# Optimization experiments

Measured on AMD Instinct MI355X. Metric: run time of the kernel, lower is better.

The kernel has to match this reference:

```python
import jax, jax.numpy as jnp
import numpy as np
import math

HIDDEN = 128; NHEADS = 4; N_COE = 50; N_SCALES = 4; THRE = 5.0; S = 4096; B = 1


def setup_inputs():
    key = jax.random.key(0)
    ks = jax.random.split(key, 12)
    w = lambda k, shape: jax.random.normal(k, shape, jnp.float32) * 0.05
    return {
        "eigenvalue": jax.random.uniform(ks[0], (B, S), jnp.float32) * 2.0,  # graph Laplacian eigvals in [0,2)
        "length": jnp.full((B,), S, dtype=jnp.int32),
        "sele_num": jnp.full((B,), S, dtype=jnp.int32),
        "eig_w_W": w(ks[1], (HIDDEN + 1, HIDDEN)), "eig_w_b": jnp.zeros((HIDDEN,), jnp.float32),
        "mha_ln_g": jnp.ones((HIDDEN,), jnp.float32), "mha_ln_b": jnp.zeros((HIDDEN,), jnp.float32),
        "in_W": w(ks[2], (HIDDEN, 3 * HIDDEN)), "in_b": jnp.zeros((3 * HIDDEN,), jnp.float32),
        "out_W": w(ks[3], (HIDDEN, HIDDEN)), "out_b": jnp.zeros((HIDDEN,), jnp.float32),
        "ffn_ln_g": jnp.ones((HIDDEN,), jnp.float32), "ffn_ln_b": jnp.zeros((HIDDEN,), jnp.float32),
        "ffn1_W": w(ks[4], (HIDDEN, HIDDEN)), "ffn1_b": jnp.zeros((HIDDEN,), jnp.float32),
        "ffn2_W": w(ks[5], (HIDDEN, HIDDEN)), "ffn2_b": jnp.zeros((HIDDEN,), jnp.float32),
        "dsc_W": w(ks[6], (HIDDEN, N_COE)), "dsc_b": jnp.zeros((N_COE,), jnp.float32),
        "dwv_W": w(ks[7], (HIDDEN, N_COE)), "dwv_b": jnp.zeros((N_COE,), jnp.float32),
        "dss_W": w(ks[8], (HIDDEN, N_SCALES)), "dss_b": jnp.zeros((N_SCALES,), jnp.float32),
    }


def layer_norm(x, g, b, eps=1e-5):
    m = x.mean(-1, keepdims=True)
    v = ((x - m) ** 2).mean(-1, keepdims=True)
    return (x - m) / jnp.sqrt(v + eps) * g + b


def sine_encoding(e, W, b):
    # e: [B, S] -> [B, S, HIDDEN]
    div = jnp.exp(jnp.arange(0, HIDDEN, 2, dtype=e.dtype) * (-math.log(10000.0) / HIDDEN))
    pe = (e * 100.0)[..., None] * div  # [B, S, HIDDEN/2]
    eeig = jnp.concatenate([e[..., None], jnp.sin(pe), jnp.cos(pe)], axis=-1)  # [B, S, HIDDEN+1]
    return eeig @ W + b


def mha(x, pad_mask, in_W, in_b, out_W, out_b):
    # x: [B, S, D]; pad_mask: [B, S] True = masked key
    Bb, Ss, D = x.shape
    hd = D // NHEADS
    qkv = x @ in_W + in_b
    q, k, v = jnp.split(qkv, 3, axis=-1)
    hsplit = lambda t: t.reshape(Bb, Ss, NHEADS, hd).transpose(0, 2, 1, 3)  # [B, H, S, hd]
    q, k, v = hsplit(q), hsplit(k), hsplit(v)
    scores = jnp.einsum('bhqd,bhkd->bhqk', q, k) / math.sqrt(hd)
    scores = jnp.where(pad_mask[:, None, None, :], -jnp.inf, scores)
    attn = jax.nn.softmax(scores, axis=-1)
    o = jnp.einsum('bhqk,bhkd->bhqd', attn, v).transpose(0, 2, 1, 3).reshape(Bb, Ss, D)
    return o @ out_W + out_b


def cheb_base(y, n_coe, flag):
    # Chebyshev recurrence: wavelet = [T_0, T_2, ...], scaling = [T_1, T_3, ...]
    te0 = jnp.ones_like(y)
    to0 = y
    def step(carry, _):
        te, to = carry
        te = 2.0 * y * to - te
        to = 2.0 * y * te - to
        return (te, to), (te, to)
    _, (evens, odds) = jax.lax.scan(step, (te0, to0), None, length=n_coe - 1)
    if flag == 'scaling':
        base = jnp.concatenate([to0[None], odds], axis=0)   # [n_coe, B, S, d]
    else:
        base = jnp.concatenate([te0[None], evens], axis=0)
    return jnp.moveaxis(base, 0, 1)  # [B, n_coe, S, d]


def _forward(eigenvalue, eig_w_W, eig_w_b, mha_ln_g, mha_ln_b, in_W, in_b, out_W, out_b,
             ffn_ln_g, ffn_ln_b, ffn1_W, ffn1_b, ffn2_W, ffn2_b,
             dsc_W, dsc_b, dwv_W, dwv_b, dss_W, dss_b, length, sele_num):
    Bb, Ss = eigenvalue.shape
    eve = eigenvalue
    eig_mask = jnp.arange(Ss)[None, :] >= sele_num[:, None]  # [B, S] True = pad
    # --- EigenEncoding (dropout in eval mode = identity) ---
    eig = sine_encoding(eve, eig_w_W, eig_w_b)
    eig = eig + mha(layer_norm(eig, mha_ln_g, mha_ln_b), eig_mask, in_W, in_b, out_W, out_b)
    f = layer_norm(eig, ffn_ln_g, ffn_ln_b)
    f = jax.nn.gelu(f @ ffn1_W + ffn1_b, approximate=False) @ ffn2_W + ffn2_b
    eig_filter = eig + f  # [B, S, HIDDEN]
    lenf = length.astype(eve.dtype)[:, None]
    def pooled(W, b):
        c = eig_filter @ W + b
        c = jnp.where(eig_mask[..., None], 0.0, c)
        return c.sum(axis=1) / (lenf + 1e-8)
    coe_scaling = jax.nn.sigmoid(pooled(dsc_W, dsc_b))
    coe_scaling = coe_scaling / (coe_scaling.sum(-1, keepdims=True) + 1e-8)  # [B, n_coe]
    coe_wavelet = jax.nn.sigmoid(pooled(dwv_W, dwv_b))
    coe_wavelet = coe_wavelet / (coe_wavelet.sum(-1, keepdims=True) + 1e-8)
    coe_scales = jax.nn.sigmoid(pooled(dss_W, dss_b)) * THRE  # [B, n_scales]
    # --- Chebyshev bases ---
    base_scaling = cheb_base(eve[..., None] - 1.0, N_COE, 'scaling')  # [B, n_coe, S, 1]
    fsw = eve[..., None] * coe_scales[:, None, :]                      # [B, S, n_scales]
    fsw = jnp.where(fsw > 2.0, 0.0, fsw)
    base_wavelet = cheb_base(fsw - 1.0, N_COE, 'wavelet')             # [B, n_coe, S, n_scales]
    base_scaling = 0.5 * (1.0 - base_scaling)
    base_wavelet = 0.5 * (1.0 - base_wavelet)
    curr_scaling = jnp.einsum('bc,bcsd->bsd', coe_scaling, base_scaling)
    curr_wavelet = jnp.einsum('bc,bcsd->bsd', coe_wavelet, base_wavelet)
    out = jnp.concatenate([curr_scaling, curr_wavelet], axis=-1)       # [B, S, 1+n_scales]
    out = out / (jnp.linalg.norm(out, axis=-1, keepdims=True) + 1e-8)  # cfg.lam.tight_use = True
    return out


def reference(eigenvalue, length, sele_num, eig_w_W, eig_w_b, mha_ln_g, mha_ln_b, in_W, in_b,
              out_W, out_b, ffn_ln_g, ffn_ln_b, ffn1_W, ffn1_b, ffn2_W, ffn2_b,
              dsc_W, dsc_b, dwv_W, dwv_b, dss_W, dss_b):
    return _forward(eigenvalue, eig_w_W, eig_w_b, mha_ln_g, mha_ln_b, in_W, in_b, out_W, out_b,
                    ffn_ln_g, ffn_ln_b, ffn1_W, ffn1_b, ffn2_W, ffn2_b,
                    dsc_W, dsc_b, dwv_W, dwv_b, dss_W, dss_b, length, sele_num)
```

## Files before the change

kernel.cpp:

```cpp
#include <hip/hip_runtime.h>
#include <hip/hip_bf16.h>
#include <math.h>


#define KSPLIT 4

typedef __attribute__((ext_vector_type(8))) short short8;
typedef __attribute__((ext_vector_type(4))) float f32x4;

__device__ inline unsigned short f2bf(float x) {
    unsigned u = __float_as_uint(x);
    return (unsigned short)((u + 0x7FFFu + ((u >> 16) & 1u)) >> 16);
}
__device__ inline float bf2f(unsigned short h) { return __uint_as_float(((unsigned)h) << 16); }
__device__ inline unsigned pk_bf16(float lo, float hi) {
    __hip_bfloat162 h = __float22bfloat162_rn(make_float2(lo, hi));
    return *reinterpret_cast<unsigned*>(&h);
}

__global__ __launch_bounds__(512) void k_embed(const float* __restrict__ eve,
    const float* __restrict__ eigW, const float* __restrict__ ebias,
    const float* __restrict__ g, const float* __restrict__ b,
    const float* __restrict__ inW, const float* __restrict__ inb,
    float* __restrict__ eig, float* __restrict__ qkv, unsigned short* __restrict__ Khi_g,
    unsigned short* __restrict__ Klo_g, unsigned short* __restrict__ Vt_g,
    float* __restrict__ xsum)
{
    __shared__ __align__(16) float wsh[2][65 * 128];
    __shared__ __align__(16) float se[16][132];
    __shared__ __align__(16) float xn[16][132];
    __shared__ __align__(16) unsigned short vsh[16][136];
    const int t = threadIdx.x;
    const int r0 = blockIdx.x * 16;
    if (blockIdx.x == 0 && t < 128) xsum[t] = 0.f;

    const float4* __restrict__ eigW4 = (const float4*)eigW;
    const float4* __restrict__ inW4  = (const float4*)inW;
    float4 pf0 = eigW4[t];
    float4 pf1 = eigW4[t + 512];
    float4 pf2 = eigW4[t + 1024];
    float4 pf3 = eigW4[t + 1536];
    float4 pf4;
    if (t < 32) pf4 = eigW4[t + 2048];

    {
        const int rr = t >> 5, l5 = t & 31;
        const float e = eve[r0 + rr];
        if (l5 == 0) se[rr][128] = e;
        #pragma unroll
        for (int jj = 0; jj < 2; ++jj) {
            const int j = l5 * 2 + jj;
            const float div = __expf(-0.07195578415606394f * (float)(2 * j));
            const float pe = e * 100.0f * div;
            se[rr][j]      = __sinf(pe);
            se[rr][64 + j] = __cosf(pe);
        }
    }
    {
        float4* dst = (float4*)wsh[0];
        dst[t] = pf0; dst[t + 512] = pf1; dst[t + 1024] = pf2; dst[t + 1536] = pf3;
        if (t < 32) dst[t + 2048] = pf4;
    }
    const int r  = t >> 5;
    const int c0 = (t & 31) * 4;
    const int kb = t >> 5, c4 = t & 31;
    float a0, a1, a2, a3;
    float xa[4];

    __syncthreads();
    pf0 = eigW4[2080 + t];        pf1 = eigW4[2080 + t + 512];
    pf2 = eigW4[2080 + t + 1024]; pf3 = eigW4[2080 + t + 1536];
    {
        const float* __restrict__ W = wsh[0];
        const float4 w0 = *(const float4*)&W[c0];
        const float ea = se[r][128];
        a0 = ea * w0.x; a1 = ea * w0.y; a2 = ea * w0.z; a3 = ea * w0.w;
        #pragma unroll 8
        for (int k = 0; k < 64; ++k) {
            const float xv = se[r][k];
            const float4 wk = *(const float4*)&W[(k + 1) * 128 + c0];
            a0 = fmaf(xv, wk.x, a0); a1 = fmaf(xv, wk.y, a1);
            a2 = fmaf(xv, wk.z, a2); a3 = fmaf(xv, wk.w, a3);
        }
    }
    {   float4* dst = (float4*)wsh[1];
        dst[t] = pf0; dst[t + 512] = pf1; dst[t + 1024] = pf2; dst[t + 1536] = pf3;
    }
    __syncthreads();
    pf0 = inW4[(size_t)(kb +  0) * 96 + c4];
    pf1 = inW4[(size_t)(kb + 16) * 96 + c4];
    pf2 = inW4[(size_t)(kb + 32) * 96 + c4];
    pf3 = inW4[(size_t)(kb + 48) * 96 + c4];
    {
        const float* __restrict__ W = wsh[1];
        #pragma unroll 8
        for (int k = 64; k < 128; ++k) {
            const float xv = se[r][k];
            const float4 wk = *(const float4*)&W[(k - 64) * 128 + c0];
            a0 = fmaf(xv, wk.x, a0); a1 = fmaf(xv, wk.y, a1);
            a2 = fmaf(xv, wk.z, a2); a3 = fmaf(xv, wk.w, a3);
        }
        const float4 bb = *(const float4*)&ebias[c0];
        xa[0] = a0 + bb.x; xa[1] = a1 + bb.y; xa[2] = a2 + bb.z; xa[3] = a3 + bb.w;
        *(float4*)&eig[(size_t)(r0 + r) * 128 + c0] = make_float4(xa[0], xa[1], xa[2], xa[3]);
        float sa = (xa[0] + xa[1]) + (xa[2] + xa[3]);
        float qa = (xa[0] * xa[0] + xa[1] * xa[1]) + (xa[2] * xa[2] + xa[3] * xa[3]);
        #pragma unroll
        for (int m = 1; m < 32; m <<= 1) {
            sa += __shfl_xor(sa, m, 32); qa += __shfl_xor(qa, m, 32);
        }
        const float ma = sa * (1.f / 128.f);
        const float ia = 1.f / sqrtf(qa * (1.f / 128.f) - ma * ma + 1e-5f);
        const float4 gg = *(const float4*)&g[c0];
        const float4 lb = *(const float4*)&b[c0];
        *(float4*)&xn[r][c0] = make_float4((xa[0] - ma) * ia * gg.x + lb.x,
                                           (xa[1] - ma) * ia * gg.y + lb.y,
                                           (xa[2] - ma) * ia * gg.z + lb.z,
                                           (xa[3] - ma) * ia * gg.w + lb.w);
    }
    {   float4* dst = (float4*)wsh[0];
        dst[t] = pf0; dst[t + 512] = pf1; dst[t + 1024] = pf2; dst[t + 1536] = pf3;
    }
    const int row = r0 + r;
    float A0, A1, A2, A3;
    #pragma unroll
    for (int p = 0; p < 3; ++p) {
        #pragma unroll
        for (int hh = 0; hh < 2; ++hh) {
            __syncthreads();
            const bool last = (p == 2 && hh == 1);
            if (!last) {
                const int np = p + hh, nh = hh ^ 1;
                pf0 = inW4[(size_t)(kb +  0 + nh * 64) * 96 + np * 32 + c4];
                pf1 = inW4[(size_t)(kb + 16 + nh * 64) * 96 + np * 32 + c4];
                pf2 = inW4[(size_t)(kb + 32 + nh * 64) * 96 + np * 32 + c4];
                pf3 = inW4[(size_t)(kb + 48 + nh * 64) * 96 + np * 32 + c4];
            }
            if (hh == 0) {
                const float4 bb = *(const float4*)&inb[p * 128 + c0];
                A0 = bb.x; A1 = bb.y; A2 = bb.z; A3 = bb.w;
            }
            const float* __restrict__ W = wsh[hh];
            #pragma unroll 8
            for (int k2 = 0; k2 < 64; ++k2) {
                const float xv = xn[r][hh * 64 + k2];
                const float4 wk = *(const float4*)&W[k2 * 128 + c0];
                A0 = fmaf(xv, wk.x, A0); A1 = fmaf(xv, wk.y, A1);
                A2 = fmaf(xv, wk.z, A2); A3 = fmaf(xv, wk.w, A3);
            }
            if (!last) {
                float4* dst = (float4*)wsh[hh ^ 1];
                dst[t] = pf0; dst[t + 512] = pf1; dst[t + 1024] = pf2; dst[t + 1536] = pf3;
            }
            if (hh == 1) {
                if (p == 0) {
                    *(float4*)&qkv[(size_t)row * 384 + c0] = make_float4(A0, A1, A2, A3);
                } else if (p == 1) {
                    const int h = c0 >> 5, d = c0 & 31;
                    float A[4] = {A0, A1, A2, A3};
                    unsigned short h4[4], l4v[4];
                    #pragma unroll
                    for (int i = 0; i < 4; ++i) { h4[i] = f2bf(A[i]); l4v[i] = f2bf(A[i] - bf2f(h4[i])); }
                    *(uint2*)&Khi_g[((size_t)h * 4096 + row) * 32 + d] = *(uint2*)h4;
                    *(uint2*)&Klo_g[((size_t)h * 4096 + row) * 32 + d] = *(uint2*)l4v;
                } else {
                    unsigned short v4[4];
                    float A[4] = {A0, A1, A2, A3};
                    #pragma unroll
                    for (int i = 0; i < 4; ++i) v4[i] = f2bf(A[i]);
                    *(uint2*)&vsh[r][c0] = *(uint2*)v4;
                }
            }
        }
    }
    __syncthreads();
    if (t < 128) {
        __align__(16) unsigned short tmp[16];
        #pragma unroll
        for (int k2 = 0; k2 < 16; ++k2) tmp[k2] = vsh[k2][t];
        *(uint4*)&Vt_g[(size_t)t * 4096 + r0]     = *(uint4*)&tmp[0];
        *(uint4*)&Vt_g[(size_t)t * 4096 + r0 + 8] = *(uint4*)&tmp[8];
    }
}

#define KSTR 40
#define VSTR 72
#define PSTR 72

__global__ __launch_bounds__(256) void k_attn(const float* __restrict__ qkv,
    const unsigned short* __restrict__ Khi_g, const unsigned short* __restrict__ Klo_g,
    const unsigned short* __restrict__ Vt_g,
    const int* __restrict__ sele, float* __restrict__ Oe, float* __restrict__ E)
{
    __shared__ __align__(16) unsigned short Khi[2][64 * KSTR];
    __shared__ __align__(16) unsigned short Klo[2][64 * KSTR];
    __shared__ __align__(16) unsigned short Vt[2][32 * VSTR];
    __shared__ __align__(16) unsigned short Pb[4][16 * PSTR];

    const int t = threadIdx.x;
    const int lane = t & 63;
    const int l = lane & 15;
    const int quad = lane >> 4;
    const int wv = __builtin_amdgcn_readfirstlane(t >> 6);
    const int qb = blockIdx.x;
    const int h  = blockIdx.y;
    const int ks = blockIdx.z;
    const int nk = sele[0];

    short8 qhi, qlo;
    {
        const float* __restrict__ qr = qkv + (size_t)(qb * 64 + wv * 16 + l) * 384 + h * 32 + quad * 8;
        const float4 a = *(const float4*)qr;
        const float4 b = *(const float4*)(qr + 4);
        const float sc = 0.17677669529663687f;
        float v[8] = {a.x * sc, a.y * sc, a.z * sc, a.w * sc, b.x * sc, b.y * sc, b.z * sc, b.w * sc};
        #pragma unroll
        for (int j = 0; j < 8; ++j) {
            const unsigned short hb = f2bf(v[j]);
            qhi[j] = (short)hb;
            qlo[j] = (short)f2bf(v[j] - bf2f(hb));
        }
    }
    f32x4 accO0 = {0.f, 0.f, 0.f, 0.f};
    f32x4 accO1 = {0.f, 0.f, 0.f, 0.f};
    float elane = 0.f;

    const int kk = t >> 2;
    const int d0 = (t & 3) * 8;
    const int vd = t >> 3;
    const int ko = (t & 7) * 8;

    const unsigned short* __restrict__ pKhi = Khi_g + ((size_t)h * 4096 + ks * 1024 + kk) * 32 + d0;
    const unsigned short* __restrict__ pKlo = Klo_g + ((size_t)h * 4096 + ks * 1024 + kk) * 32 + d0;
    const unsigned short* __restrict__ pVt  = Vt_g  + ((size_t)h * 32 + vd) * 4096 + ks * 1024 + ko;

    uint4 kh_n = *(const uint4*)pKhi;
    uint4 kl_n = *(const uint4*)pKlo;
    uint4 vv_n = *(const uint4*)pVt;
    *(uint4*)&Khi[0][kk * KSTR + d0] = kh_n;
    *(uint4*)&Klo[0][kk * KSTR + d0] = kl_n;
    *(uint4*)&Vt[0][vd * VSTR + ko]  = vv_n;

    for (int ch = 0; ch < 16; ++ch) {
        __syncthreads();
        const int cur = ch & 1;
        if (ch < 15) {
            kh_n = *(const uint4*)(pKhi + (size_t)(ch + 1) * 2048);
            kl_n = *(const uint4*)(pKlo + (size_t)(ch + 1) * 2048);
            vv_n = *(const uint4*)(pVt  + (ch + 1) * 64);
        }
        const int keybase = ks * 1024 + ch * 64;
        const unsigned short* __restrict__ KhiC = Khi[cur];
        const unsigned short* __restrict__ KloC = Klo[cur];
        const unsigned short* __restrict__ VtC  = Vt[cur];
        unsigned short* __restrict__ Pw = Pb[wv];
        #pragma unroll
        for (int tile = 0; tile < 4; ++tile) {
            const int kl = tile * 16 + l;
            const short8 kh = *(const short8*)&KhiC[kl * KSTR + quad * 8];
            const short8 kw = *(const short8*)&KloC[kl * KSTR + quad * 8];
            f32x4 S = {0.f, 0.f, 0.f, 0.f};
            __builtin_amdgcn_s_setprio(1);
            S = __builtin_amdgcn_mfma_f32_16x16x32_bf16(kh, qhi, S, 0, 0, 0);
            S = __builtin_amdgcn_mfma_f32_16x16x32_bf16(kw, qhi, S, 0, 0, 0);
            S = __builtin_amdgcn_mfma_f32_16x16x32_bf16(kh, qlo, S, 0, 0, 0);
            __builtin_amdgcn_s_setprio(0);
            const int kg0 = keybase + tile * 16 + quad * 4;
            const float p0 = (kg0 + 0 < nk) ? __expf(S[0]) : 0.f;
            const float p1 = (kg0 + 1 < nk) ? __expf(S[1]) : 0.f;
            const float p2 = (kg0 + 2 < nk) ? __expf(S[2]) : 0.f;
            const float p3 = (kg0 + 3 < nk) ? __expf(S[3]) : 0.f;
            elane += (p0 + p1) + (p2 + p3);
            *(uint2*)&Pw[l * PSTR + tile * 16 + quad * 4] =
                make_uint2(pk_bf16(p0, p1), pk_bf16(p2, p3));
        }
        #pragma unroll
        for (int step = 0; step < 2; ++step) {
            const short8 pa  = *(const short8*)&Pw[l * PSTR + step * 32 + quad * 8];
            const short8 vb0 = *(const short8*)&VtC[l * VSTR + step * 32 + quad * 8];
            const short8 vb1 = *(const short8*)&VtC[(16 + l) * VSTR + step * 32 + quad * 8];
            __builtin_amdgcn_s_setprio(1);
            accO0 = __builtin_amdgcn_mfma_f32_16x16x32_bf16(pa, vb0, accO0, 0, 0, 0);
            accO1 = __builtin_amdgcn_mfma_f32_16x16x32_bf16(pa, vb1, accO1, 0, 0, 0);
            __builtin_amdgcn_s_setprio(0);
        }
        if (ch < 15) {
            *(uint4*)&Khi[cur ^ 1][kk * KSTR + d0] = kh_n;
            *(uint4*)&Klo[cur ^ 1][kk * KSTR + d0] = kl_n;
            *(uint4*)&Vt[cur ^ 1][vd * VSTR + ko]  = vv_n;
        }
    }
    elane += __shfl_xor(elane, 16, 64);
    elane += __shfl_xor(elane, 32, 64);
    const int qrow0 = qb * 64 + wv * 16;
    if (lane < 16)
        E[((size_t)ks * 4 + h) * 4096 + qrow0 + l] = elane;
    #pragma unroll
    for (int r = 0; r < 4; ++r) {
        const size_t row = qrow0 + quad * 4 + r;
        Oe[((size_t)ks * 4096 + row) * 128 + h * 32 + l]      = accO0[r];
        Oe[((size_t)ks * 4096 + row) * 128 + h * 32 + 16 + l] = accO1[r];
    }
}

__global__ __launch_bounds__(512) void k_ffn(const float* __restrict__ eig,
    const float* __restrict__ Oe, const float* __restrict__ E,
    const float* __restrict__ outW, const float* __restrict__ outb,
    const float* __restrict__ lg, const float* __restrict__ lb,
    const float* __restrict__ W1, const float* __restrict__ b1,
    const float* __restrict__ W2, const float* __restrict__ b2,
    const int* __restrict__ sele, float* __restrict__ xsum)
{
    __shared__ __align__(16) float wsh[2][64 * 128];
    __shared__ __align__(16) float sA[16][132];
    __shared__ __align__(16) float xn[16][132];
    __shared__ __align__(16) float cs[16][132];
    const int t = threadIdx.x;
    const int r0 = blockIdx.x * 16;
    const int r  = t >> 5;
    const int c0 = (t & 31) * 4;

    const float4* __restrict__ Wp0 = (const float4*)outW;
    const float4* __restrict__ Wp1 = (const float4*)W1;
    const float4* __restrict__ Wp2 = (const float4*)W2;

    float4 pf0 = Wp0[t], pf1 = Wp0[t + 512], pf2 = Wp0[t + 1024], pf3 = Wp0[t + 1536];

    {
        const int h = c0 >> 5;
        float es = 0.f;
        float v[4] = {0.f, 0.f, 0.f, 0.f};
        #pragma unroll
        for (int ks = 0; ks < KSPLIT; ++ks) {
            es += E[((size_t)ks * 4 + h) * 4096 + r0 + r];
            const float4 o1 = *(const float4*)&Oe[((size_t)ks * 4096 + r0 + r) * 128 + c0];
            v[0] += o1.x; v[1] += o1.y; v[2] += o1.z; v[3] += o1.w;
        }
        const float rcp = 1.f / es;
        *(float4*)&sA[r][c0] = make_float4(v[0] * rcp, v[1] * rcp, v[2] * rcp, v[3] * rcp);
    }
    {   float4* dst = (float4*)wsh[0];
        dst[t] = pf0; dst[t + 512] = pf1; dst[t + 1024] = pf2; dst[t + 1536] = pf3;
    }

    float x2[4];
    float A0, A1, A2, A3;
    #pragma unroll
    for (int gphase = 0; gphase < 6; ++gphase) {
        const int gg = gphase >> 1, hh = gphase & 1;
        __syncthreads();
        if (gphase < 5) {
            const int nid = gphase + 1;
            const int ng = nid >> 1, nh = nid & 1;
            const float4* __restrict__ src = (ng == 0) ? Wp0 : (ng == 1 ? Wp1 : Wp2);
            pf0 = src[nh * 2048 + t];        pf1 = src[nh * 2048 + t + 512];
            pf2 = src[nh * 2048 + t + 1024]; pf3 = src[nh * 2048 + t + 1536];
        }
        if (hh == 0) {
            const float* bias = (gg == 0) ? outb : (gg == 1 ? b1 : b2);
            const float4 bb = *(const float4*)&bias[c0];
            A0 = bb.x; A1 = bb.y; A2 = bb.z; A3 = bb.w;
        }
        const float* __restrict__ W = wsh[hh];
        const float* __restrict__ act = (gg == 1) ? &xn[r][0] : &sA[r][0];
        #pragma unroll 8
        for (int k2 = 0; k2 < 64; ++k2) {
            const float xv = act[hh * 64 + k2];
            const float4 wk = *(const float4*)&W[k2 * 128 + c0];
            A0 = fmaf(xv, wk.x, A0); A1 = fmaf(xv, wk.y, A1);
            A2 = fmaf(xv, wk.z, A2); A3 = fmaf(xv, wk.w, A3);
        }
        if (gphase < 5) {
            float4* dst = (float4*)wsh[hh ^ 1];
            dst[t] = pf0; dst[t + 512] = pf1; dst[t + 1024] = pf2; dst[t + 1536] = pf3;
        }
        if (hh == 1) {
            if (gg == 0) {
                const float4 ea = *(const float4*)&eig[(size_t)(r0 + r) * 128 + c0];
                x2[0] = ea.x + A0; x2[1] = ea.y + A1; x2[2] = ea.z + A2; x2[3] = ea.w + A3;
                float sa = (x2[0] + x2[1]) + (x2[2] + x2[3]);
                float qa = (x2[0] * x2[0] + x2[1] * x2[1]) + (x2[2] * x2[2] + x2[3] * x2[3]);
                #pragma unroll
                for (int m = 1; m < 32; m <<= 1) {
                    sa += __shfl_xor(sa, m, 32); qa += __shfl_xor(qa, m, 32);
                }
                const float ma = sa * (1.f / 128.f);
                const float ia = 1.f / sqrtf(qa * (1.f / 128.f) - ma * ma + 1e-5f);
                const float4 gg4 = *(const float4*)&lg[c0];
                const float4 bb4 = *(const float4*)&lb[c0];
                *(float4*)&xn[r][c0] = make_float4((x2[0] - ma) * ia * gg4.x + bb4.x,
                                                   (x2[1] - ma) * ia * gg4.y + bb4.y,
                                                   (x2[2] - ma) * ia * gg4.z + bb4.z,
                                                   (x2[3] - ma) * ia * gg4.w + bb4.w);
            } else if (gg == 1) {
                *(float4*)&sA[r][c0] = make_float4(
                    0.5f * A0 * (1.f + erff(A0 * 0.70710678118654752f)),
                    0.5f * A1 * (1.f + erff(A1 * 0.70710678118654752f)),
                    0.5f * A2 * (1.f + erff(A2 * 0.70710678118654752f)),
                    0.5f * A3 * (1.f + erff(A3 * 0.70710678118654752f)));
            } else {
                const int nsel = sele[0];
                const bool ina = (r0 + r) < nsel;
                *(float4*)&cs[r][c0] = ina ? make_float4(x2[0] + A0, x2[1] + A1, x2[2] + A2, x2[3] + A3)
                                           : make_float4(0.f, 0.f, 0.f, 0.f);
            }
        }
    }
    __syncthreads();
    if (t < 128) {
        float s = 0.f;
        #pragma unroll
        for (int rr = 0; rr < 16; ++rr) s += cs[rr][t];
        atomicAdd(&xsum[t], s);
    }
}

__global__ __launch_bounds__(128) void k_tail(const float* __restrict__ eve,
    const float* __restrict__ xsum,
    const float* __restrict__ dscW, const float* __restrict__ dscb,
    const float* __restrict__ dwvW, const float* __restrict__ dwvb,
    const float* __restrict__ dssW, const float* __restrict__ dssb,
    const int* __restrict__ len, const int* __restrict__ sele,
    float* __restrict__ out)
{
    __shared__ float xs[128];
    __shared__ float val[104];
    __shared__ float s2[2];
    __shared__ float csc[50], cwv[50], cssh[4];
    const int t = threadIdx.x;
    xs[t] = xsum[t];
    __syncthreads();
    if (t < 104) {
        const float invl = 1.f / ((float)len[0] + 1e-8f);
        const float ns = (float)sele[0];
        const float* Wp; int stride, col; float bias;
        if (t < 50)       { Wp = dscW; stride = 50; col = t;       bias = dscb[t]; }
        else if (t < 100) { Wp = dwvW; stride = 50; col = t - 50;  bias = dwvb[t - 50]; }
        else              { Wp = dssW; stride = 4;  col = t - 100; bias = dssb[t - 100]; }
        float a = 0.f;
        #pragma unroll 4
        for (int k = 0; k < 128; ++k) a = fmaf(xs[k], Wp[k * stride + col], a);
        a = (a + ns * bias) * invl;
        val[t] = 1.f / (1.f + __expf(-a));
    }
    __syncthreads();
    if (t == 0) { float s = 0.f; for (int i = 0; i < 50; ++i) s += val[i]; s2[0] = s; }
    if (t == 1) { float s = 0.f; for (int i = 0; i < 50; ++i) s += val[50 + i]; s2[1] = s; }
    __syncthreads();
    if (t < 50) {
        csc[t] = val[t] / (s2[0] + 1e-8f);
        cwv[t] = val[50 + t] / (s2[1] + 1e-8f);
    } else if (t >= 100 && t < 104) {
        cssh[t - 100] = val[t] * 5.0f;
    }
    __syncthreads();
    const int s = blockIdx.x * 128 + t;
    const float e = eve[s];
    float vals[5];
    {
        const float y = e - 1.f;
        float te = 1.f, to = y;
        float a = csc[0] * (0.5f * (1.f - to));
        const float y2 = 2.f * y;
        for (int i = 1; i < 50; ++i) {
            te = fmaf(y2, to, -te);
            to = fmaf(y2, te, -to);
            a = fmaf(csc[i], 0.5f * (1.f - to), a);
        }
        vals[0] = a;
    }
    #pragma unroll
    for (int j = 0; j < 4; ++j) {
        float f = e * cssh[j];
        if (f > 2.f) f = 0.f;
        const float y = f - 1.f;
        float te = 1.f, to = y;
        float a = cwv[0] * (0.5f * (1.f - te));
        const float y2 = 2.f * y;
        for (int i = 1; i < 50; ++i) {
            te = fmaf(y2, to, -te);
            to = fmaf(y2, te, -to);
            a = fmaf(cwv[i], 0.5f * (1.f - te), a);
        }
        vals[1 + j] = a;
    }
    float n2 = 0.f;
    #pragma unroll
    for (int k = 0; k < 5; ++k) n2 += vals[k] * vals[k];
    const float invn = 1.f / (sqrtf(n2) + 1e-8f);
    #pragma unroll
    for (int k = 0; k < 5; ++k) out[s * 5 + k] = vals[k] * invn;
}

extern "C" void kernel_launch(void* const* d_in, const int* in_sizes, int n_in,
                              void* d_out, int out_size, void* d_ws, size_t ws_size,
                              hipStream_t stream) {
    const float* eve  = (const float*)d_in[0];
    const int*   len  = (const int*)d_in[1];
    const int*   sele = (const int*)d_in[2];
    const float* eigW = (const float*)d_in[3];
    const float* eigB = (const float*)d_in[4];
    const float* mlg  = (const float*)d_in[5];
    const float* mlb  = (const float*)d_in[6];
    const float* inW  = (const float*)d_in[7];
    const float* inb  = (const float*)d_in[8];
    const float* outW = (const float*)d_in[9];
    const float* outb = (const float*)d_in[10];
    const float* flg  = (const float*)d_in[11];
    const float* flb  = (const float*)d_in[12];
    const float* W1   = (const float*)d_in[13];
    const float* b1   = (const float*)d_in[14];
    const float* W2   = (const float*)d_in[15];
    const float* b2   = (const float*)d_in[16];
    const float* dscW = (const float*)d_in[17];
    const float* dscb = (const float*)d_in[18];
    const float* dwvW = (const float*)d_in[19];
    const float* dwvb = (const float*)d_in[20];
    const float* dssW = (const float*)d_in[21];
    const float* dssb = (const float*)d_in[22];

    float* ws   = (float*)d_ws;
    float* eig  = ws;
    float* qkv  = ws + 524288;
    float* Oe   = ws + 2097152;
    float* E    = ws + 4194304;
    float* xsum = ws + 4259840;
    unsigned short* Khi_g = (unsigned short*)(ws + 4260352);
    unsigned short* Klo_g = (unsigned short*)(ws + 4522496);
    unsigned short* Vt_g  = (unsigned short*)(ws + 4784640);
    float* out  = (float*)d_out;

    k_embed<<<256, 512, 0, stream>>>(eve, eigW, eigB, mlg, mlb, inW, inb,
                                     eig, qkv, Khi_g, Klo_g, Vt_g, xsum);
    k_attn <<<dim3(64, 4, KSPLIT), 256, 0, stream>>>(qkv, Khi_g, Klo_g, Vt_g, sele, Oe, E);
    k_ffn  <<<256, 512, 0, stream>>>(eig, Oe, E, outW, outb, flg, flb, W1, b1, W2, b2, sele, xsum);
    k_tail <<<32, 128, 0, stream>>>(eve, xsum, dscW, dscb, dwvW, dwvb, dssW, dssb, len, sele, out);
}
```

Baseline: 180.6 us.

## Compute two rows per thread in embed/FFN GEMVs and spread tail over more blocks

k_embed and k_ffn drop from 512 to 256 threads per block, and each thread now accumulates two rows. Every shared-memory weight float4 load is reused for two rows, which halves LDS weight traffic per FMA, at the cost of more registers and fewer waves. k_tail goes from 32 to 256 blocks, and each thread now computes one of the five Chebyshev series for one eigenvalue instead of all five. This spreads the serial 50-step recurrences across many more threads, but every block repeats the small coefficient MLP prologue.

```diff
diff --git a/kernel.cpp b/kernel.cpp
--- a/kernel.cpp
+++ b/kernel.cpp
@@ -18,7 +18,7 @@
     return *reinterpret_cast<unsigned*>(&h);
 }
 
-__global__ __launch_bounds__(512) void k_embed(const float* __restrict__ eve,
+__global__ __launch_bounds__(256) void k_embed(const float* __restrict__ eve,
     const float* __restrict__ eigW, const float* __restrict__ ebias,
     const float* __restrict__ g, const float* __restrict__ b,
     const float* __restrict__ inW, const float* __restrict__ inb,
@@ -36,20 +36,18 @@
 
     const float4* __restrict__ eigW4 = (const float4*)eigW;
     const float4* __restrict__ inW4  = (const float4*)inW;
-    float4 pf0 = eigW4[t];
-    float4 pf1 = eigW4[t + 512];
-    float4 pf2 = eigW4[t + 1024];
-    float4 pf3 = eigW4[t + 1536];
-    float4 pf4;
-    if (t < 32) pf4 = eigW4[t + 2048];
+    float4 pf[8]; float4 pfx;
+    #pragma unroll
+    for (int i = 0; i < 8; ++i) pf[i] = eigW4[t + i * 256];
+    if (t < 32) pfx = eigW4[t + 2048];
 
     {
-        const int rr = t >> 5, l5 = t & 31;
+        const int rr = t >> 4, l4 = t & 15;
         const float e = eve[r0 + rr];
-        if (l5 == 0) se[rr][128] = e;
-        #pragma unroll
-        for (int jj = 0; jj < 2; ++jj) {
-            const int j = l5 * 2 + jj;
+        if (l4 == 0) se[rr][128] = e;
+        #pragma unroll
+        for (int jj = 0; jj < 4; ++jj) {
+            const int j = l4 * 4 + jj;
             const float div = __expf(-0.07195578415606394f * (float)(2 * j));
             const float pe = e * 100.0f * div;
             se[rr][j]      = __sinf(pe);
@@ -58,71 +56,92 @@
     }
     {
         float4* dst = (float4*)wsh[0];
-        dst[t] = pf0; dst[t + 512] = pf1; dst[t + 1024] = pf2; dst[t + 1536] = pf3;
-        if (t < 32) dst[t + 2048] = pf4;
-    }
-    const int r  = t >> 5;
-    const int c0 = (t & 31) * 4;
+        #pragma unroll
+        for (int i = 0; i < 8; ++i) dst[t + i * 256] = pf[i];
+        if (t < 32) dst[t + 2048] = pfx;
+    }
+    const int lane = t & 63;
+    const int w = t >> 6;
+    const int rp = w * 2 + (lane >> 5);
+    const int c0 = (lane & 31) * 4;
+    const int ra = rp * 2, rb = ra + 1;
     const int kb = t >> 5, c4 = t & 31;
-    float a0, a1, a2, a3;
-    float xa[4];
-
-    __syncthreads();
-    pf0 = eigW4[2080 + t];        pf1 = eigW4[2080 + t + 512];
-    pf2 = eigW4[2080 + t + 1024]; pf3 = eigW4[2080 + t + 1536];
+    float a0, a1, a2, a3, b0, b1, b2, b3;
+    float xa[4], xb[4];
+
+    __syncthreads();
+    #pragma unroll
+    for (int i = 0; i < 8; ++i) pf[i] = eigW4[2080 + t + i * 256];
     {
         const float* __restrict__ W = wsh[0];
         const float4 w0 = *(const float4*)&W[c0];
-        const float ea = se[r][128];
+        const float ea = se[ra][128], eb = se[rb][128];
         a0 = ea * w0.x; a1 = ea * w0.y; a2 = ea * w0.z; a3 = ea * w0.w;
+        b0 = eb * w0.x; b1 = eb * w0.y; b2 = eb * w0.z; b3 = eb * w0.w;
         #pragma unroll 8
         for (int k = 0; k < 64; ++k) {
-            const float xv = se[r][k];
+            const float xva = se[ra][k];
+            const float xvb = se[rb][k];
             const float4 wk = *(const float4*)&W[(k + 1) * 128 + c0];
-            a0 = fmaf(xv, wk.x, a0); a1 = fmaf(xv, wk.y, a1);
-            a2 = fmaf(xv, wk.z, a2); a3 = fmaf(xv, wk.w, a3);
+            a0 = fmaf(xva, wk.x, a0); a1 = fmaf(xva, wk.y, a1);
+            a2 = fmaf(xva, wk.z, a2); a3 = fmaf(xva, wk.w, a3);
+            b0 = fmaf(xvb, wk.x, b0); b1 = fmaf(xvb, wk.y, b1);
+            b2 = fmaf(xvb, wk.z, b2); b3 = fmaf(xvb, wk.w, b3);
         }
     }
     {   float4* dst = (float4*)wsh[1];
-        dst[t] = pf0; dst[t + 512] = pf1; dst[t + 1024] = pf2; dst[t + 1536] = pf3;
-    }
-    __syncthreads();
-    pf0 = inW4[(size_t)(kb +  0) * 96 + c4];
-    pf1 = inW4[(size_t)(kb + 16) * 96 + c4];
-    pf2 = inW4[(size_t)(kb + 32) * 96 + c4];
-    pf3 = inW4[(size_t)(kb + 48) * 96 + c4];
+        #pragma unroll
+        for (int i = 0; i < 8; ++i) dst[t + i * 256] = pf[i];
+    }
+    __syncthreads();
+    #pragma unroll
+    for (int i = 0; i < 8; ++i) pf[i] = inW4[(size_t)(kb + 8 * i) * 96 + c4];
     {
         const float* __restrict__ W = wsh[1];
         #pragma unroll 8
-        for (int k = 64; k < 128; ++k) {
-            const float xv = se[r][k];
-            const float4 wk = *(const float4*)&W[(k - 64) * 128 + c0];
-            a0 = fmaf(xv, wk.x, a0); a1 = fmaf(xv, wk.y, a1);
-            a2 = fmaf(xv, wk.z, a2); a3 = fmaf(xv, wk.w, a3);
+        for (int k2 = 0; k2 < 64; ++k2) {
+            const float xva = se[ra][64 + k2];
+            const float xvb = se[rb][64 + k2];
+            const float4 wk = *(const float4*)&W[k2 * 128 + c0];
+            a0 = fmaf(xva, wk.x, a0); a1 = fmaf(xva, wk.y, a1);
+            a2 = fmaf(xva, wk.z, a2); a3 = fmaf(xva, wk.w, a3);
+            b0 = fmaf(xvb, wk.x, b0); b1 = fmaf(xvb, wk.y, b1);
+            b2 = fmaf(xvb, wk.z, b2); b3 = fmaf(xvb, wk.w, b3);
         }
         const float4 bb = *(const float4*)&ebias[c0];
         xa[0] = a0 + bb.x; xa[1] = a1 + bb.y; xa[2] = a2 + bb.z; xa[3] = a3 + bb.w;
-        *(float4*)&eig[(size_t)(r0 + r) * 128 + c0] = make_float4(xa[0], xa[1], xa[2], xa[3]);
+        xb[0] = b0 + bb.x; xb[1] = b1 + bb.y; xb[2] = b2 + bb.z; xb[3] = b3 + bb.w;
+        *(float4*)&eig[(size_t)(r0 + ra) * 128 + c0] = make_float4(xa[0], xa[1], xa[2], xa[3]);
+        *(float4*)&eig[(size_t)(r0 + rb) * 128 + c0] = make_float4(xb[0], xb[1], xb[2], xb[3]);
         float sa = (xa[0] + xa[1]) + (xa[2] + xa[3]);
         float qa = (xa[0] * xa[0] + xa[1] * xa[1]) + (xa[2] * xa[2] + xa[3] * xa[3]);
+        float sb = (xb[0] + xb[1]) + (xb[2] + xb[3]);
+        float qb = (xb[0] * xb[0] + xb[1] * xb[1]) + (xb[2] * xb[2] + xb[3] * xb[3]);
         #pragma unroll
         for (int m = 1; m < 32; m <<= 1) {
             sa += __shfl_xor(sa, m, 32); qa += __shfl_xor(qa, m, 32);
-        }
-        const float ma = sa * (1.f / 128.f);
+            sb += __shfl_xor(sb, m, 32); qb += __shfl_xor(qb, m, 32);
+        }
+        const float ma = sa * (1.f / 128.f), mb = sb * (1.f / 128.f);
         const float ia = 1.f / sqrtf(qa * (1.f / 128.f) - ma * ma + 1e-5f);
+        const float ib = 1.f / sqrtf(qb * (1.f / 128.f) - mb * mb + 1e-5f);
         const float4 gg = *(const float4*)&g[c0];
         const float4 lb = *(const float4*)&b[c0];
-        *(float4*)&xn[r][c0] = make_float4((xa[0] - ma) * ia * gg.x + lb.x,
-                                           (xa[1] - ma) * ia * gg.y + lb.y,
-                                           (xa[2] - ma) * ia * gg.z + lb.z,
-                                           (xa[3] - ma) * ia * gg.w + lb.w);
+        *(float4*)&xn[ra][c0] = make_float4((xa[0] - ma) * ia * gg.x + lb.x,
+                                            (xa[1] - ma) * ia * gg.y + lb.y,
+                                            (xa[2] - ma) * ia * gg.z + lb.z,
+                                            (xa[3] - ma) * ia * gg.w + lb.w);
+        *(float4*)&xn[rb][c0] = make_float4((xb[0] - mb) * ib * gg.x + lb.x,
+                                            (xb[1] - mb) * ib * gg.y + lb.y,
+                                            (xb[2] - mb) * ib * gg.z + lb.z,
+                                            (xb[3] - mb) * ib * gg.w + lb.w);
     }
     {   float4* dst = (float4*)wsh[0];
-        dst[t] = pf0; dst[t + 512] = pf1; dst[t + 1024] = pf2; dst[t + 1536] = pf3;
-    }
-    const int row = r0 + r;
-    float A0, A1, A2, A3;
+        #pragma unroll
+        for (int i = 0; i < 8; ++i) dst[t + i * 256] = pf[i];
+    }
+    const int rowa = r0 + ra, rowb = r0 + rb;
+    float A[4], Bv[4];
     #pragma unroll
     for (int p = 0; p < 3; ++p) {
         #pragma unroll
@@ -131,44 +150,54 @@
             const bool last = (p == 2 && hh == 1);
             if (!last) {
                 const int np = p + hh, nh = hh ^ 1;
-                pf0 = inW4[(size_t)(kb +  0 + nh * 64) * 96 + np * 32 + c4];
-                pf1 = inW4[(size_t)(kb + 16 + nh * 64) * 96 + np * 32 + c4];
-                pf2 = inW4[(size_t)(kb + 32 + nh * 64) * 96 + np * 32 + c4];
-                pf3 = inW4[(size_t)(kb + 48 + nh * 64) * 96 + np * 32 + c4];
+                #pragma unroll
+                for (int i = 0; i < 8; ++i)
+                    pf[i] = inW4[(size_t)(kb + 8 * i + nh * 64) * 96 + np * 32 + c4];
             }
             if (hh == 0) {
                 const float4 bb = *(const float4*)&inb[p * 128 + c0];
-                A0 = bb.x; A1 = bb.y; A2 = bb.z; A3 = bb.w;
+                A[0] = bb.x; A[1] = bb.y; A[2] = bb.z; A[3] = bb.w;
+                Bv[0] = bb.x; Bv[1] = bb.y; Bv[2] = bb.z; Bv[3] = bb.w;
             }
             const float* __restrict__ W = wsh[hh];
             #pragma unroll 8
             for (int k2 = 0; k2 < 64; ++k2) {
-                const float xv = xn[r][hh * 64 + k2];
+                const float xva = xn[ra][hh * 64 + k2];
+                const float xvb = xn[rb][hh * 64 + k2];
                 const float4 wk = *(const float4*)&W[k2 * 128 + c0];
-                A0 = fmaf(xv, wk.x, A0); A1 = fmaf(xv, wk.y, A1);
-                A2 = fmaf(xv, wk.z, A2); A3 = fmaf(xv, wk.w, A3);
+                A[0] = fmaf(xva, wk.x, A[0]); A[1] = fmaf(xva, wk.y, A[1]);
+                A[2] = fmaf(xva, wk.z, A[2]); A[3] = fmaf(xva, wk.w, A[3]);
+                Bv[0] = fmaf(xvb, wk.x, Bv[0]); Bv[1] = fmaf(xvb, wk.y, Bv[1]);
+                Bv[2] = fmaf(xvb, wk.z, Bv[2]); Bv[3] = fmaf(xvb, wk.w, Bv[3]);
             }
             if (!last) {
                 float4* dst = (float4*)wsh[hh ^ 1];
-                dst[t] = pf0; dst[t + 512] = pf1; dst[t + 1024] = pf2; dst[t + 1536] = pf3;
+                #pragma unroll
+                for (int i = 0; i < 8; ++i) dst[t + i * 256] = pf[i];
             }
             if (hh == 1) {
                 if (p == 0) {
-                    *(float4*)&qkv[(size_t)row * 384 + c0] = make_float4(A0, A1, A2, A3);
+                    *(float4*)&qkv[(size_t)rowa * 384 + c0] = make_float4(A[0], A[1], A[2], A[3]);
+                    *(float4*)&qkv[(size_t)rowb * 384 + c0] = make_float4(Bv[0], Bv[1], Bv[2], Bv[3]);
                 } else if (p == 1) {
                     const int h = c0 >> 5, d = c0 & 31;
-                    float A[4] = {A0, A1, A2, A3};
                     unsigned short h4[4], l4v[4];
                     #pragma unroll
                     for (int i = 0; i < 4; ++i) { h4[i] = f2bf(A[i]); l4v[i] = f2bf(A[i] - bf2f(h4[i])); }
-                    *(uint2*)&Khi_g[((size_t)h * 4096 + row) * 32 + d] = *(uint2*)h4;
-                    *(uint2*)&Klo_g[((size_t)h * 4096 + row) * 32 + d] = *(uint2*)l4v;
+                    *(uint2*)&Khi_g[((size_t)h * 4096 + rowa) * 32 + d] = *(uint2*)h4;
+                    *(uint2*)&Klo_g[((size_t)h * 4096 + rowa) * 32 + d] = *(uint2*)l4v;
+                    #pragma unroll
+                    for (int i = 0; i < 4; ++i) { h4[i] = f2bf(Bv[i]); l4v[i] = f2bf(Bv[i] - bf2f(h4[i])); }
+                    *(uint2*)&Khi_g[((size_t)h * 4096 + rowb) * 32 + d] = *(uint2*)h4;
+                    *(uint2*)&Klo_g[((size_t)h * 4096 + rowb) * 32 + d] = *(uint2*)l4v;
                 } else {
                     unsigned short v4[4];
-                    float A[4] = {A0, A1, A2, A3};
                     #pragma unroll
                     for (int i = 0; i < 4; ++i) v4[i] = f2bf(A[i]);
-                    *(uint2*)&vsh[r][c0] = *(uint2*)v4;
+                    *(uint2*)&vsh[ra][c0] = *(uint2*)v4;
+                    #pragma unroll
+                    for (int i = 0; i < 4; ++i) v4[i] = f2bf(Bv[i]);
+                    *(uint2*)&vsh[rb][c0] = *(uint2*)v4;
                 }
             }
         }
@@ -303,7 +332,7 @@
     }
 }
 
-__global__ __launch_bounds__(512) void k_ffn(const float* __restrict__ eig,
+__global__ __launch_bounds__(256) void k_ffn(const float* __restrict__ eig,
     const float* __restrict__ Oe, const float* __restrict__ E,
     const float* __restrict__ outW, const float* __restrict__ outb,
     const float* __restrict__ lg, const float* __restrict__ lb,
@@ -317,34 +346,44 @@
     __shared__ __align__(16) float cs[16][132];
     const int t = threadIdx.x;
     const int r0 = blockIdx.x * 16;
-    const int r  = t >> 5;
-    const int c0 = (t & 31) * 4;
+    const int lane = t & 63;
+    const int w = t >> 6;
+    const int rp = w * 2 + (lane >> 5);
+    const int c0 = (lane & 31) * 4;
+    const int ra = rp * 2, rb = ra + 1;
 
     const float4* __restrict__ Wp0 = (const float4*)outW;
     const float4* __restrict__ Wp1 = (const float4*)W1;
     const float4* __restrict__ Wp2 = (const float4*)W2;
 
-    float4 pf0 = Wp0[t], pf1 = Wp0[t + 512], pf2 = Wp0[t + 1024], pf3 = Wp0[t + 1536];
+    float4 pf[8];
+    #pragma unroll
+    for (int i = 0; i < 8; ++i) pf[i] = Wp0[t + i * 256];
 
     {
-        const int h = c0 >> 5;
+        const int r = t >> 4, c8 = (t & 15) * 8;
+        const int h = c8 >> 5;
         float es = 0.f;
-        float v[4] = {0.f, 0.f, 0.f, 0.f};
+        float v[8] = {0.f, 0.f, 0.f, 0.f, 0.f, 0.f, 0.f, 0.f};
         #pragma unroll
         for (int ks = 0; ks < KSPLIT; ++ks) {
             es += E[((size_t)ks * 4 + h) * 4096 + r0 + r];
-            const float4 o1 = *(const float4*)&Oe[((size_t)ks * 4096 + r0 + r) * 128 + c0];
+            const float4 o1 = *(const float4*)&Oe[((size_t)ks * 4096 + r0 + r) * 128 + c8];
+            const float4 o2 = *(const float4*)&Oe[((size_t)ks * 4096 + r0 + r) * 128 + c8 + 4];
             v[0] += o1.x; v[1] += o1.y; v[2] += o1.z; v[3] += o1.w;
+            v[4] += o2.x; v[5] += o2.y; v[6] += o2.z; v[7] += o2.w;
         }
         const float rcp = 1.f / es;
-        *(float4*)&sA[r][c0] = make_float4(v[0] * rcp, v[1] * rcp, v[2] * rcp, v[3] * rcp);
+        *(float4*)&sA[r][c8]     = make_float4(v[0] * rcp, v[1] * rcp, v[2] * rcp, v[3] * rcp);
+        *(float4*)&sA[r][c8 + 4] = make_float4(v[4] * rcp, v[5] * rcp, v[6] * rcp, v[7] * rcp);
     }
     {   float4* dst = (float4*)wsh[0];
-        dst[t] = pf0; dst[t + 512] = pf1; dst[t + 1024] = pf2; dst[t + 1536] = pf3;
-    }
-
-    float x2[4];
-    float A0, A1, A2, A3;
+        #pragma unroll
+        for (int i = 0; i < 8; ++i) dst[t + i * 256] = pf[i];
+    }
+
+    float x2a[4], x2b[4];
+    float A[4], Bv[4];
     #pragma unroll
     for (int gphase = 0; gphase < 6; ++gphase) {
         const int gg = gphase >> 1, hh = gphase & 1;
@@ -353,56 +392,81 @@
             const int nid = gphase + 1;
             const int ng = nid >> 1, nh = nid & 1;
             const float4* __restrict__ src = (ng == 0) ? Wp0 : (ng == 1 ? Wp1 : Wp2);
-            pf0 = src[nh * 2048 + t];        pf1 = src[nh * 2048 + t + 512];
-            pf2 = src[nh * 2048 + t + 1024]; pf3 = src[nh * 2048 + t + 1536];
+            #pragma unroll
+            for (int i = 0; i < 8; ++i) pf[i] = src[nh * 2048 + t + i * 256];
         }
         if (hh == 0) {
             const float* bias = (gg == 0) ? outb : (gg == 1 ? b1 : b2);
             const float4 bb = *(const float4*)&bias[c0];
-            A0 = bb.x; A1 = bb.y; A2 = bb.z; A3 = bb.w;
+            A[0] = bb.x; A[1] = bb.y; A[2] = bb.z; A[3] = bb.w;
+            Bv[0] = bb.x; Bv[1] = bb.y; Bv[2] = bb.z; Bv[3] = bb.w;
         }
         const float* __restrict__ W = wsh[hh];
-        const float* __restrict__ act = (gg == 1) ? &xn[r][0] : &sA[r][0];
+        const float* __restrict__ actA = (gg == 1) ? &xn[ra][0] : &sA[ra][0];
+        const float* __restrict__ actB = (gg == 1) ? &xn[rb][0] : &sA[rb][0];
         #pragma unroll 8
         for (int k2 = 0; k2 < 64; ++k2) {
-            const float xv = act[hh * 64 + k2];
+            const float xva = actA[hh * 64 + k2];
+            const float xvb = actB[hh * 64 + k2];
             const float4 wk = *(const float4*)&W[k2 * 128 + c0];
-            A0 = fmaf(xv, wk.x, A0); A1 = fmaf(xv, wk.y, A1);
-            A2 = fmaf(xv, wk.z, A2); A3 = fmaf(xv, wk.w, A3);
+            A[0] = fmaf(xva, wk.x, A[0]); A[1] = fmaf(xva, wk.y, A[1]);
+            A[2] = fmaf(xva, wk.z, A[2]); A[3] = fmaf(xva, wk.w, A[3]);
+            Bv[0] = fmaf(xvb, wk.x, Bv[0]); Bv[1] = fmaf(xvb, wk.y, Bv[1]);
+            Bv[2] = fmaf(xvb, wk.z, Bv[2]); Bv[3] = fmaf(xvb, wk.w, Bv[3]);
         }
         if (gphase < 5) {
             float4* dst = (float4*)wsh[hh ^ 1];
-            dst[t] = pf0; dst[t + 512] = pf1; dst[t + 1024] = pf2; dst[t + 1536] = pf3;
+            #pragma unroll
+            for (int i = 0; i < 8; ++i) dst[t + i * 256] = pf[i];
         }
         if (hh == 1) {
             if (gg == 0) {
-                const float4 ea = *(const float4*)&eig[(size_t)(r0 + r) * 128 + c0];
-                x2[0] = ea.x + A0; x2[1] = ea.y + A1; x2[2] = ea.z + A2; x2[3] = ea.w + A3;
-                float sa = (x2[0] + x2[1]) + (x2[2] + x2[3]);
-                float qa = (x2[0] * x2[0] + x2[1] * x2[1]) + (x2[2] * x2[2] + x2[3] * x2[3]);
+                const float4 ea = *(const float4*)&eig[(size_t)(r0 + ra) * 128 + c0];
+                const float4 eb = *(const float4*)&eig[(size_t)(r0 + rb) * 128 + c0];
+                x2a[0] = ea.x + A[0]; x2a[1] = ea.y + A[1]; x2a[2] = ea.z + A[2]; x2a[3] = ea.w + A[3];
+                x2b[0] = eb.x + Bv[0]; x2b[1] = eb.y + Bv[1]; x2b[2] = eb.z + Bv[2]; x2b[3] = eb.w + Bv[3];
+                float sa = (x2a[0] + x2a[1]) + (x2a[2] + x2a[3]);
+                float qa = (x2a[0] * x2a[0] + x2a[1] * x2a[1]) + (x2a[2] * x2a[2] + x2a[3] * x2a[3]);
+                float sb = (x2b[0] + x2b[1]) + (x2b[2] + x2b[3]);
+                float qb = (x2b[0] * x2b[0] + x2b[1] * x2b[1]) + (x2b[2] * x2b[2] + x2b[3] * x2b[3]);
                 #pragma unroll
                 for (int m = 1; m < 32; m <<= 1) {
                     sa += __shfl_xor(sa, m, 32); qa += __shfl_xor(qa, m, 32);
+                    sb += __shfl_xor(sb, m, 32); qb += __shfl_xor(qb, m, 32);
                 }
-                const float ma = sa * (1.f / 128.f);
+                const float ma = sa * (1.f / 128.f), mb = sb * (1.f / 128.f);
                 const float ia = 1.f / sqrtf(qa * (1.f / 128.f) - ma * ma + 1e-5f);
+                const float ib = 1.f / sqrtf(qb * (1.f / 128.f) - mb * mb + 1e-5f);
                 const float4 gg4 = *(const float4*)&lg[c0];
                 const float4 bb4 = *(const float4*)&lb[c0];
-                *(float4*)&xn[r][c0] = make_float4((x2[0] - ma) * ia * gg4.x + bb4.x,
-                                                   (x2[1] - ma) * ia * gg4.y + bb4.y,
-                                                   (x2[2] - ma) * ia * gg4.z + bb4.z,
-                                                   (x2[3] - ma) * ia * gg4.w + bb4.w);
+                *(float4*)&xn[ra][c0] = make_float4((x2a[0] - ma) * ia * gg4.x + bb4.x,
+                                                    (x2a[1] - ma) * ia * gg4.y + bb4.y,
+                                                    (x2a[2] - ma) * ia * gg4.z + bb4.z,
+                                                    (x2a[3] - ma) * ia * gg4.w + bb4.w);
+                *(float4*)&xn[rb][c0] = make_float4((x2b[0] - mb) * ib * gg4.x + bb4.x,
+                                                    (x2b[1] - mb) * ib * gg4.y + bb4.y,
+                                                    (x2b[2] - mb) * ib * gg4.z + bb4.z,
+                                                    (x2b[3] - mb) * ib * gg4.w + bb4.w);
             } else if (gg == 1) {
-                *(float4*)&sA[r][c0] = make_float4(
-                    0.5f * A0 * (1.f + erff(A0 * 0.70710678118654752f)),
-                    0.5f * A1 * (1.f + erff(A1 * 0.70710678118654752f)),
-                    0.5f * A2 * (1.f + erff(A2 * 0.70710678118654752f)),
-                    0.5f * A3 * (1.f + erff(A3 * 0.70710678118654752f)));
+                *(float4*)&sA[ra][c0] = make_float4(
+                    0.5f * A[0] * (1.f + erff(A[0] * 0.70710678118654752f)),
+                    0.5f * A[1] * (1.f + erff(A[1] * 0.70710678118654752f)),
+                    0.5f * A[2] * (1.f + erff(A[2] * 0.70710678118654752f)),
+                    0.5f * A[3] * (1.f + erff(A[3] * 0.70710678118654752f)));
+                *(float4*)&sA[rb][c0] = make_float4(
+                    0.5f * Bv[0] * (1.f + erff(Bv[0] * 0.70710678118654752f)),
+                    0.5f * Bv[1] * (1.f + erff(Bv[1] * 0.70710678118654752f)),
+                    0.5f * Bv[2] * (1.f + erff(Bv[2] * 0.70710678118654752f)),
+                    0.5f * Bv[3] * (1.f + erff(Bv[3] * 0.70710678118654752f)));
             } else {
                 const int nsel = sele[0];
-                const bool ina = (r0 + r) < nsel;
-                *(float4*)&cs[r][c0] = ina ? make_float4(x2[0] + A0, x2[1] + A1, x2[2] + A2, x2[3] + A3)
-                                           : make_float4(0.f, 0.f, 0.f, 0.f);
+                const bool ina = (r0 + ra) < nsel, inb2 = (r0 + rb) < nsel;
+                *(float4*)&cs[ra][c0] = ina ? make_float4(x2a[0] + A[0], x2a[1] + A[1],
+                                                          x2a[2] + A[2], x2a[3] + A[3])
+                                            : make_float4(0.f, 0.f, 0.f, 0.f);
+                *(float4*)&cs[rb][c0] = inb2 ? make_float4(x2b[0] + Bv[0], x2b[1] + Bv[1],
+                                                           x2b[2] + Bv[2], x2b[3] + Bv[3])
+                                             : make_float4(0.f, 0.f, 0.f, 0.f);
             }
         }
     }
@@ -427,6 +491,7 @@
     __shared__ float val[104];
     __shared__ float s2[2];
     __shared__ float csc[50], cwv[50], cssh[4];
+    __shared__ float sv[16][6];
     const int t = threadIdx.x;
     xs[t] = xsum[t];
     __syncthreads();
@@ -454,42 +519,33 @@
         cssh[t - 100] = val[t] * 5.0f;
     }
     __syncthreads();
-    const int s = blockIdx.x * 128 + t;
-    const float e = eve[s];
-    float vals[5];
-    {
-        const float y = e - 1.f;
+    const int e_i = t / 5, c = t - e_i * 5;
+    if (t < 80) {
+        const float e = eve[blockIdx.x * 16 + e_i];
+        float y;
+        if (c == 0) y = e - 1.f;
+        else { float f = e * cssh[c - 1]; if (f > 2.f) f = 0.f; y = f - 1.f; }
+        const float* __restrict__ cf = (c == 0) ? csc : cwv;
         float te = 1.f, to = y;
-        float a = csc[0] * (0.5f * (1.f - to));
+        float u = (c == 0) ? to : te;
+        float a = cf[0] * (0.5f * (1.f - u));
         const float y2 = 2.f * y;
         for (int i = 1; i < 50; ++i) {
             te = fmaf(y2, to, -te);
             to = fmaf(y2, te, -to);
-            a = fmaf(csc[i], 0.5f * (1.f - to), a);
-        }
-        vals[0] = a;
-    }
-    #pragma unroll
-    for (int j = 0; j < 4; ++j) {
-        float f = e * cssh[j];
-        if (f > 2.f) f = 0.f;
-        const float y = f - 1.f;
-        float te = 1.f, to = y;
-        float a = cwv[0] * (0.5f * (1.f - te));
-        const float y2 = 2.f * y;
-        for (int i = 1; i < 50; ++i) {
-            te = fmaf(y2, to, -te);
-            to = fmaf(y2, te, -to);
-            a = fmaf(cwv[i], 0.5f * (1.f - te), a);
-        }
-        vals[1 + j] = a;
-    }
-    float n2 = 0.f;
-    #pragma unroll
-    for (int k = 0; k < 5; ++k) n2 += vals[k] * vals[k];
-    const float invn = 1.f / (sqrtf(n2) + 1e-8f);
-    #pragma unroll
-    for (int k = 0; k < 5; ++k) out[s * 5 + k] = vals[k] * invn;
+            u = (c == 0) ? to : te;
+            a = fmaf(cf[i], 0.5f * (1.f - u), a);
+        }
+        sv[e_i][c] = a;
+    }
+    __syncthreads();
+    if (t < 80) {
+        float n2 = 0.f;
+        #pragma unroll
+        for (int k = 0; k < 5; ++k) n2 += sv[e_i][k] * sv[e_i][k];
+        const float invn = 1.f / (sqrtf(n2) + 1e-8f);
+        out[(size_t)(blockIdx.x * 16 + e_i) * 5 + c] = sv[e_i][c] * invn;
+    }
 }
 
 extern "C" void kernel_launch(void* const* d_in, const int* in_sizes, int n_in,
@@ -530,9 +586,9 @@
     unsigned short* Vt_g  = (unsigned short*)(ws + 4784640);
     float* out  = (float*)d_out;
 
-    k_embed<<<256, 512, 0, stream>>>(eve, eigW, eigB, mlg, mlb, inW, inb,
+    k_embed<<<256, 256, 0, stream>>>(eve, eigW, eigB, mlg, mlb, inW, inb,
                                      eig, qkv, Khi_g, Klo_g, Vt_g, xsum);
     k_attn <<<dim3(64, 4, KSPLIT), 256, 0, stream>>>(qkv, Khi_g, Klo_g, Vt_g, sele, Oe, E);
-    k_ffn  <<<256, 512, 0, stream>>>(eig, Oe, E, outW, outb, flg, flb, W1, b1, W2, b2, sele, xsum);
-    k_tail <<<32, 128, 0, stream>>>(eve, xsum, dscW, dscb, dwvW, dwvb, dssW, dssb, len, sele, out);
-}
+    k_ffn  <<<256, 256, 0, stream>>>(eig, Oe, E, outW, outb, flg, flb, W1, b1, W2, b2, sele, xsum);
+    k_tail <<<256, 128, 0, stream>>>(eve, xsum, dscW, dscb, dwvW, dwvb, dssW, dssb, len, sele, out);
+}
```

Result: slower. 188.3 us (+4.3%).
